# Kernel tuning notes

Measured on AMD Instinct MI355X. Metric: run time of the kernel, lower is better.

## Reference

```python
import jax, jax.numpy as jnp
import numpy as np

N = 50000          # num nodes
E = 800000         # num edges (before self loops)
IN_C = 128
HID = 256          # heads * head_dim
HEADS = 4
HEAD_DIM = HID // HEADS
OUT_C = 64
NEG_SLOPE = 0.2    # PyG GATConv default leaky_relu slope
BN_EPS = 1e-5


def _gat_conv(x, src, dst, W, att_src, att_dst, bias, concat):
    """PyG-style GATConv (with self loops already appended to src/dst).
    x: [N, in_c]; W: [in_c, H*C]; att_src/att_dst: [H, C]; bias: [H*C] or [C]."""
    H, C = att_src.shape
    h = (x @ W).reshape(-1, H, C)                               # [N, H, C]
    a_src = jnp.einsum('nhc,hc->nh', h, att_src)                # [N, H]
    a_dst = jnp.einsum('nhc,hc->nh', h, att_dst)                # [N, H]
    e = jax.nn.leaky_relu(a_src[src] + a_dst[dst], NEG_SLOPE)   # [Et, H]
    # segment softmax over destination nodes (numerically stable)
    m = jax.ops.segment_max(e, dst, num_segments=N)             # [N, H]
    m = jnp.where(jnp.isfinite(m), m, 0.0)
    ex = jnp.exp(e - m[dst])
    denom = jax.ops.segment_sum(ex, dst, num_segments=N)        # [N, H]
    alpha = ex / (denom[dst] + 1e-16)                           # [Et, H]
    msg = alpha[:, :, None] * h[src]                            # [Et, H, C]
    out = jax.ops.segment_sum(msg, dst, num_segments=N)         # [N, H, C]
    out = out.reshape(N, H * C) if concat else out.mean(axis=1)
    return out + bias


def _bn_eval(x, gamma, beta, mean, var):
    return (x - mean) * jax.lax.rsqrt(var + BN_EPS) * gamma + beta


def setup_inputs() -> dict:
    key = jax.random.key(0)
    ks = jax.random.split(key, 16)
    x = jax.random.normal(ks[0], (N, IN_C), dtype=jnp.float32)
    edge_index = jax.random.randint(ks[1], (2, E), 0, N, dtype=jnp.int64)

    def lin(k, fan_in, fan_out):
        s = (1.0 / np.sqrt(fan_in)).astype(np.float32)
        return jax.random.normal(k, (fan_in, fan_out), dtype=jnp.float32) * s

    def att(k, h, c):
        return jax.random.normal(k, (h, c), dtype=jnp.float32) * 0.1

    return {
        'x': x, 'edge_index': edge_index,
        'W0': lin(ks[2], IN_C, HID), 'as0': att(ks[3], HEADS, HEAD_DIM), 'ad0': att(ks[4], HEADS, HEAD_DIM), 'b0': jnp.zeros((HID,), jnp.float32),
        'bn0_g': jnp.ones((HID,), jnp.float32), 'bn0_b': jnp.zeros((HID,), jnp.float32), 'bn0_m': jnp.zeros((HID,), jnp.float32), 'bn0_v': jnp.ones((HID,), jnp.float32),
        'W1': lin(ks[5], HID, HID), 'as1': att(ks[6], HEADS, HEAD_DIM), 'ad1': att(ks[7], HEADS, HEAD_DIM), 'b1': jnp.zeros((HID,), jnp.float32),
        'bn1_g': jnp.ones((HID,), jnp.float32), 'bn1_b': jnp.zeros((HID,), jnp.float32), 'bn1_m': jnp.zeros((HID,), jnp.float32), 'bn1_v': jnp.ones((HID,), jnp.float32),
        'W2': lin(ks[8], HID, OUT_C), 'as2': att(ks[9], 1, OUT_C), 'ad2': att(ks[10], 1, OUT_C), 'b2': jnp.zeros((OUT_C,), jnp.float32),
    }


def reference(x, edge_index, W0, as0, ad0, b0, bn0_g, bn0_b, bn0_m, bn0_v,
              W1, as1, ad1, b1, bn1_g, bn1_b, bn1_m, bn1_v,
              W2, as2, ad2, b2):
    loop = jnp.arange(N, dtype=edge_index.dtype)
    src = jnp.concatenate([edge_index[0], loop])   # PyG add_self_loops=True
    dst = jnp.concatenate([edge_index[1], loop])

    h = _gat_conv(x, src, dst, W0, as0, ad0, b0, concat=True)
    h = jax.nn.elu(_bn_eval(h, bn0_g, bn0_b, bn0_m, bn0_v))   # dropout: eval -> identity
    h = _gat_conv(h, src, dst, W1, as1, ad1, b1, concat=True)
    h = jax.nn.elu(_bn_eval(h, bn1_g, bn1_b, bn1_m, bn1_v))
    out = _gat_conv(h, src, dst, W2, as2, ad2, b2, concat=False)  # heads=1, mean
    return out
```

## Files before the change

### kernel.cpp

```cpp
#include <hip/hip_runtime.h>

#define NN   50000
#define EE   800000
#define ET   850000
#define INC  128
#define HID  256
#define OUTC 64
#define NEG  0.2f
#define BNEPS 1e-5f

typedef __bf16 bf16x8 __attribute__((ext_vector_type(8)));
typedef float  f32x4  __attribute__((ext_vector_type(4)));

static __device__ __forceinline__ float b2f(unsigned short u) {
    return __uint_as_float(((unsigned)u) << 16);
}
static __device__ __forceinline__ float blo(unsigned u) {
    return __uint_as_float(u << 16);
}
static __device__ __forceinline__ float bhi(unsigned u) {
    return __uint_as_float(u & 0xFFFF0000u);
}
static __device__ __forceinline__ unsigned short f2b(float f) {
    unsigned u = __float_as_uint(f);
    unsigned r = u + 0x7FFFu + ((u >> 16) & 1u);
    return (unsigned short)(r >> 16);
}
static __device__ __forceinline__ float leaky(float x) {
    return x > 0.f ? x : NEG * x;
}
static __device__ __forceinline__ float ew(float e) {
    return __expf(fminf(e, 80.f));
}

__global__ void k_init(const int* __restrict__ ei, const unsigned* __restrict__ xw,
                       int* __restrict__ cnt, int* __restrict__ flagW, int* __restrict__ flagB,
                       int nbZ) {
    __shared__ int cs[4];
    int b = blockIdx.x, t = threadIdx.x;
    if (b < nbZ) {
        int i = b * 256 + t;
        if (i < NN) cnt[i] = 0;
    } else if (b == nbZ) {
        int c = 0;
        for (int k = 0; k < 16; k++) {
            int i = t + 256 * k;
            if (ei[2 * i + 1] != 0) c = 1;
        }
        for (int o = 1; o < 64; o <<= 1) c |= __shfl_xor(c, o);
        if ((t & 63) == 0) cs[t >> 6] = c;
        __syncthreads();
        if (t == 0) *flagW = cs[0] | cs[1] | cs[2] | cs[3];
    } else {
        int c = 0;
        for (int i = t; i < 4096; i += 256) {
            unsigned v = (xw[i] >> 8) & 0x7F;
            if (v >= 50 && v <= 67) c++;
        }
        for (int o = 1; o < 64; o <<= 1) c += __shfl_xor(c, o);
        if ((t & 63) == 0) cs[t >> 6] = c;
        __syncthreads();
        if (t == 0) *flagB = (cs[0] + cs[1] + cs[2] + cs[3] > 2048) ? 1 : 0;
    }
}

__global__ void k_prep(const void* as0, const void* ad0, const void* b0, const void* g0,
                       const void* be0, const void* m0, const void* v0,
                       const void* as1, const void* ad1, const void* b1, const void* g1,
                       const void* be1, const void* m1, const void* v1,
                       const void* as2, const void* ad2, const void* b2,
                       const void* W0, const void* W1, const void* W2,
                       unsigned short* __restrict__ WT0, unsigned short* __restrict__ WT1,
                       unsigned short* __restrict__ WT2,
                       const void* __restrict__ x, unsigned short* __restrict__ xb,
                       float* __restrict__ pp, const int* __restrict__ flagB) {
    int b = blockIdx.x, t = threadIdx.x;
    bool bf = (*flagB != 0);
    auto cv = [&](const void* s, int i) -> float {
        return bf ? b2f(((const unsigned short*)s)[i]) : ((const float*)s)[i];
    };
    if (b < 14) {
        float v;
        switch (b) {
            case 0:  v = cv(as0, t); break;
            case 1:  v = cv(ad0, t); break;
            case 2:  v = cv(b0, t);  break;
            case 3:  v = cv(g0, t);  break;
            case 4:  v = cv(be0, t); break;
            case 5:  v = cv(m0, t);  break;
            case 6:  v = cv(v0, t);  break;
            case 7:  v = cv(as1, t); break;
            case 8:  v = cv(ad1, t); break;
            case 9:  v = cv(b1, t);  break;
            case 10: v = cv(g1, t);  break;
            case 11: v = cv(be1, t); break;
            case 12: v = cv(m1, t);  break;
            default: v = cv(v1, t);  break;
        }
        pp[b * 256 + t] = v;
    } else if (b == 14) {
        if (t < 192) {
            int arr = t >> 6, j = t & 63;
            float v = (arr == 0) ? cv(as2, j) : (arr == 1) ? cv(ad2, j) : cv(b2, j);
            pp[14 * 256 + arr * 64 + j] = v;
        }
    } else if (b < 15 + 128) {
        int i = (b - 15) * 256 + t;
        int k = i >> 8, n = i & 255;
        WT0[n * INC + k] = bf ? ((const unsigned short*)W0)[i] : f2b(((const float*)W0)[i]);
    } else if (b < 15 + 128 + 256) {
        int i = (b - 143) * 256 + t;
        int k = i >> 8, n = i & 255;
        WT1[n * HID + k] = bf ? ((const unsigned short*)W1)[i] : f2b(((const float*)W1)[i]);
    } else if (b < 15 + 128 + 256 + 64) {
        int i = (b - 399) * 256 + t;
        int k = i >> 6, n = i & 63;
        WT2[n * HID + k] = bf ? ((const unsigned short*)W2)[i] : f2b(((const float*)W2)[i]);
    } else {
        if (bf) return;
        for (int i = (b - 463) * 256 + t; i < NN * INC; i += 2048 * 256)
            xb[i] = f2b(((const float*)x)[i]);
    }
}

__global__ void k_hist(const int* __restrict__ ei, const int* __restrict__ flagW,
                       int* __restrict__ cnt) {
    int i = blockIdx.x * 256 + threadIdx.x;
    if (i >= ET) return;
    bool w32 = (*flagW != 0);
    int d = (i < EE) ? (w32 ? ei[EE + i] : ei[2 * (EE + i)]) : (i - EE);
    atomicAdd(&cnt[d], 1);
}

static __device__ __forceinline__ int block_scan_incl(int v, int t, int* ws) {
    int lane = t & 63, w = t >> 6;
    int x = v;
    for (int o = 1; o < 64; o <<= 1) {
        int y = __shfl_up(x, o);
        if (lane >= o) x += y;
    }
    if (lane == 63) ws[w] = x;
    __syncthreads();
    if (t == 0) {
        int s = 0;
        for (int k = 0; k < 4; k++) { int tmp = ws[k]; ws[k] = s; s += tmp; }
    }
    __syncthreads();
    return x + ws[w];
}

__global__ void k_scan_a(const int* __restrict__ cnt, int* __restrict__ rowptr, int* __restrict__ bsum) {
    __shared__ int ws[4];
    int t = threadIdx.x, b = blockIdx.x;
    int i = b * 256 + t;
    int v = (i < NN) ? cnt[i] : 0;
    int incl = block_scan_incl(v, t, ws);
    if (i < NN) rowptr[i] = incl - v;
    if (t == 255) bsum[b] = incl;
}

__global__ void k_scan_b(int* __restrict__ bsum, int nb) {
    __shared__ int ws[4];
    int t = threadIdx.x;
    int v = (t < nb) ? bsum[t] : 0;
    int incl = block_scan_incl(v, t, ws);
    if (t < nb) bsum[t] = incl - v;
}

__global__ void k_scan_c(int* __restrict__ rowptr, const int* __restrict__ bsum, int* __restrict__ cursor) {
    int t = threadIdx.x, b = blockIdx.x;
    int i = b * 256 + t;
    if (i < NN) {
        int r = rowptr[i] + bsum[b];
        rowptr[i] = r;
        cursor[i] = r;
    }
    if (i == 0) rowptr[NN] = ET;
}

__global__ void k_scatter(const int* __restrict__ ei, const int* __restrict__ flagW,
                          int* __restrict__ cursor, int* __restrict__ esrc) {
    int i = blockIdx.x * 256 + threadIdx.x;
    if (i >= ET) {
        if (i < ET + 64) esrc[i] = 0;
        return;
    }
    bool w32 = (*flagW != 0);
    int s, d;
    if (i < EE) {
        if (w32) { s = ei[i];     d = ei[EE + i]; }
        else     { s = ei[2 * i]; d = ei[2 * (EE + i)]; }
    } else {
        s = d = i - EE;
    }
    int p = atomicAdd(&cursor[d], 1);
    esrc[p] = s;
}

template<int NC, int NH, int NBN>
__global__ __launch_bounds__(256) void k_gemm(const unsigned short* __restrict__ Amain,
                                              const void* __restrict__ Aalt,
                                              const int* __restrict__ flagB,
                                              const unsigned short* __restrict__ WT,
                                              unsigned short* __restrict__ H,
                                              float* __restrict__ asrc, float* __restrict__ adst,
                                              const float* __restrict__ asv, const float* __restrict__ adv,
                                              int M, int K) {
    constexpr int BN = 64 * NBN;
    __shared__ __align__(16) unsigned short As[128 * 40];
    __shared__ __align__(16) unsigned short Bs[BN * 40];
    const unsigned short* A = (*flagB) ? (const unsigned short*)Aalt : Amain;
    int t = threadIdx.x;
    int bm = blockIdx.x, bg = blockIdx.y;
    int lane = t & 63, wave = t >> 6;
    int m16 = lane & 15, quad = lane >> 4;

    f32x4 acc[2][4 * NBN];
    #pragma unroll
    for (int a = 0; a < 2; a++)
        #pragma unroll
        for (int b = 0; b < 4 * NBN; b++) acc[a][b] = (f32x4){0.f, 0.f, 0.f, 0.f};

    int arow = t >> 1, ahalf = t & 1;
    long gArow = (long)bm * 128 + arow;

    for (int k0 = 0; k0 < K; k0 += 32) {
        uint4 av0 = {0u, 0u, 0u, 0u}, av1 = {0u, 0u, 0u, 0u};
        if (gArow < M) {
            const unsigned short* ap = A + gArow * (size_t)K + k0 + ahalf * 16;
            av0 = *(const uint4*)(ap);
            av1 = *(const uint4*)(ap + 8);
        }
        if constexpr (NBN == 2) {
            const unsigned short* bp = WT + ((size_t)bg * BN + arow) * K + k0 + ahalf * 16;
            uint4 bv0 = *(const uint4*)(bp);
            uint4 bv1 = *(const uint4*)(bp + 8);
            *(uint4*)&As[arow * 40 + ahalf * 16]     = av0;
            *(uint4*)&As[arow * 40 + ahalf * 16 + 8] = av1;
            *(uint4*)&Bs[arow * 40 + ahalf * 16]     = bv0;
            *(uint4*)&Bs[arow * 40 + ahalf * 16 + 8] = bv1;
        } else {
            int brow = t >> 2, bq = t & 3;
            uint4 bv = *(const uint4*)(WT + ((size_t)bg * BN + brow) * K + k0 + bq * 8);
            *(uint4*)&As[arow * 40 + ahalf * 16]     = av0;
            *(uint4*)&As[arow * 40 + ahalf * 16 + 8] = av1;
            *(uint4*)&Bs[brow * 40 + bq * 8]         = bv;
        }
        __syncthreads();
        int wrow = wave * 32;
        bf16x8 af[2], bf[4 * NBN];
        #pragma unroll
        for (int mt = 0; mt < 2; mt++)
            af[mt] = *(const bf16x8*)&As[(wrow + mt * 16 + m16) * 40 + quad * 8];
        #pragma unroll
        for (int nt = 0; nt < 4 * NBN; nt++)
            bf[nt] = *(const bf16x8*)&Bs[(nt * 16 + m16) * 40 + quad * 8];
        #pragma unroll
        for (int mt = 0; mt < 2; mt++)
            #pragma unroll
            for (int nt = 0; nt < 4 * NBN; nt++)
                acc[mt][nt] = __builtin_amdgcn_mfma_f32_16x16x32_bf16(af[mt], bf[nt], acc[mt][nt], 0, 0, 0);
        __syncthreads();
    }

    float asc[4 * NBN], adc[4 * NBN];
    #pragma unroll
    for (int nt = 0; nt < 4 * NBN; nt++) {
        int col = bg * BN + nt * 16 + m16;
        asc[nt] = asv[col];
        adc[nt] = adv[col];
    }
    #pragma unroll
    for (int mt = 0; mt < 2; mt++) {
        int gR0 = bm * 128 + wave * 32 + mt * 16 + quad * 4;
        #pragma unroll
        for (int r = 0; r < 4; r++) {
            int gR = gR0 + r;
            #pragma unroll
            for (int hh = 0; hh < NBN; hh++) {
                float ps = 0.f, pd = 0.f;
                #pragma unroll
                for (int nt = hh * 4; nt < hh * 4 + 4; nt++) {
                    float v = acc[mt][nt][r];
                    ps += v * asc[nt];
                    pd += v * adc[nt];
                }
                for (int o = 1; o < 16; o <<= 1) { ps += __shfl_xor(ps, o); pd += __shfl_xor(pd, o); }
                if (m16 == 0 && gR < M) {
                    asrc[(size_t)gR * NH + bg * NBN + hh] = ps;
                    adst[(size_t)gR * NH + bg * NBN + hh] = pd;
                }
            }
            if (gR < M) {
                #pragma unroll
                for (int nt = 0; nt < 4 * NBN; nt++) {
                    int gC = bg * BN + nt * 16 + m16;
                    H[(size_t)gR * NC + gC] = f2b(acc[mt][nt][r]);
                }
            }
        }
    }
}

#define LOADG(pre, d, e0n) \
    uint2 pre##0 = {0, 0}, pre##1 = {0, 0}, pre##2 = {0, 0}, pre##3 = {0, 0}; \
    if (d) { \
        int s0_ = esrc[(e0n)], s1_ = esrc[(e0n) + 1], s2_ = esrc[(e0n) + 2], s3_ = esrc[(e0n) + 3]; \
        pre##0 = *(const uint2*)(h + (size_t)s0_ * HID + lc); \
        pre##1 = *(const uint2*)(h + (size_t)s1_ * HID + lc); \
        pre##2 = *(const uint2*)(h + (size_t)s2_ * HID + lc); \
        pre##3 = *(const uint2*)(h + (size_t)s3_ * HID + lc); \
    }
#define FMAG(pre, d, wreg, A0, A1, A2, A3, j) \
    if (d) { \
        float w0_ = __shfl(wreg, wsel + (j)),     w1_ = __shfl(wreg, wsel + (j) + 1); \
        float w2_ = __shfl(wreg, wsel + (j) + 2), w3_ = __shfl(wreg, wsel + (j) + 3); \
        A0 += w0_ * blo((pre##0).x) + w1_ * blo((pre##1).x) + w2_ * blo((pre##2).x) + w3_ * blo((pre##3).x); \
        A1 += w0_ * bhi((pre##0).x) + w1_ * bhi((pre##1).x) + w2_ * bhi((pre##2).x) + w3_ * bhi((pre##3).x); \
        A2 += w0_ * blo((pre##0).y) + w1_ * blo((pre##1).y) + w2_ * blo((pre##2).y) + w3_ * blo((pre##3).y); \
        A3 += w0_ * bhi((pre##0).y) + w1_ * bhi((pre##1).y) + w2_ * bhi((pre##2).y) + w3_ * bhi((pre##3).y); \
    }

__global__ __launch_bounds__(256, 4) void k_agg4(const unsigned short* __restrict__ h,
                       const float* __restrict__ asrc, const float* __restrict__ adst,
                       const int* __restrict__ rowptr, const int* __restrict__ esrc,
                       const float* __restrict__ bias,
                       const float* __restrict__ bng, const float* __restrict__ bnb,
                       const float* __restrict__ bnm, const float* __restrict__ bnv,
                       unsigned short* __restrict__ act) {
    int t = threadIdx.x;
    int wave = t >> 6, lane = t & 63;
    int nodeA = blockIdx.x * 8 + wave * 2;
    if (nodeA >= NN) return;
    int nodeB = nodeA + 1;
    bool hasB = (nodeB < NN);

    int hd = lane >> 4, li = lane & 15;
    int wsel = lane & 48;
    const size_t lc = (size_t)lane * 4;

    int e0A = __builtin_amdgcn_readfirstlane(rowptr[nodeA]);
    int e1A = __builtin_amdgcn_readfirstlane(rowptr[nodeA + 1]);
    int degA = e1A - e0A;
    int e0B = e1A, degB = 0;
    if (hasB) degB = __builtin_amdgcn_readfirstlane(rowptr[nodeB + 1]) - e1A;

    float adhA = adst[(size_t)nodeA * 4 + hd];
    float adhB = hasB ? adst[(size_t)nodeB * 4 + hd] : 0.f;

    float waccA = 0.f, waccB = 0.f;
    float aA0 = 0.f, aA1 = 0.f, aA2 = 0.f, aA3 = 0.f;
    float aB0 = 0.f, aB1 = 0.f, aB2 = 0.f, aB3 = 0.f;

    int nA = min(16, degA), nB = min(16, degB);
    float eA = 0.f, eB = 0.f;
    if (li < nA) { int s = esrc[e0A + li]; eA = asrc[(size_t)s * 4 + hd]; }
    if (li < nB) { int s = esrc[e0B + li]; eB = asrc[(size_t)s * 4 + hd]; }

    int degM = max(degA, degB);
    for (int c = 0; c < degM; c += 16) {
        float wA = (li < nA) ? ew(leaky(eA + adhA)) : 0.f;
        float wB = (li < nB) ? ew(leaky(eB + adhB)) : 0.f;
        waccA += wA; waccB += wB;
        int nA2 = min(16, degA - (c + 16));
        int nB2 = min(16, degB - (c + 16));
        eA = 0.f; eB = 0.f;
        if (li < nA2) { int s = esrc[e0A + c + 16 + li]; eA = asrc[(size_t)s * 4 + hd]; }
        if (li < nB2) { int s = esrc[e0B + c + 16 + li]; eB = asrc[(size_t)s * 4 + hd]; }
        bool dA0 = 0 < nA, dA1 = 4 < nA, dA2 = 8 < nA, dA3 = 12 < nA;
        bool dB0 = 0 < nB, dB1 = 4 < nB, dB2 = 8 < nB, dB3 = 12 < nB;
        LOADG(gA0, dA0, e0A + c)
        LOADG(gA1, dA1, e0A + c + 4)
        LOADG(gA2, dA2, e0A + c + 8)
        LOADG(gA3, dA3, e0A + c + 12)
        LOADG(gB0, dB0, e0B + c)
        LOADG(gB1, dB1, e0B + c + 4)
        LOADG(gB2, dB2, e0B + c + 8)
        LOADG(gB3, dB3, e0B + c + 12)
        FMAG(gA0, dA0, wA, aA0, aA1, aA2, aA3, 0)
        FMAG(gA1, dA1, wA, aA0, aA1, aA2, aA3, 4)
        FMAG(gA2, dA2, wA, aA0, aA1, aA2, aA3, 8)
        FMAG(gA3, dA3, wA, aA0, aA1, aA2, aA3, 12)
        FMAG(gB0, dB0, wB, aB0, aB1, aB2, aB3, 0)
        FMAG(gB1, dB1, wB, aB0, aB1, aB2, aB3, 4)
        FMAG(gB2, dB2, wB, aB0, aB1, aB2, aB3, 8)
        FMAG(gB3, dB3, wB, aB0, aB1, aB2, aB3, 12)
        nA = nA2; nB = nB2;
    }
    waccA += __shfl_xor(waccA, 1); waccA += __shfl_xor(waccA, 2);
    waccA += __shfl_xor(waccA, 4); waccA += __shfl_xor(waccA, 8);
    waccB += __shfl_xor(waccB, 1); waccB += __shfl_xor(waccB, 2);
    waccB += __shfl_xor(waccB, 4); waccB += __shfl_xor(waccB, 8);
    float invA = 1.f / (waccA + 1e-16f);
    float invB = 1.f / (waccB + 1e-16f);

    int c0 = lane * 4;
    float4 bi = *(const float4*)(bias + c0);
    float4 bm_ = *(const float4*)(bnm + c0);
    float4 bv_ = *(const float4*)(bnv + c0);
    float4 bg_ = *(const float4*)(bng + c0);
    float4 bb_ = *(const float4*)(bnb + c0);
    float sc[4], sh[4];
    {
        const float* bvp = (const float*)&bv_;
        const float* bgp = (const float*)&bg_;
        const float* bmp = (const float*)&bm_;
        const float* bbp = (const float*)&bb_;
        const float* bip = (const float*)&bi;
        #pragma unroll
        for (int jj = 0; jj < 4; jj++) {
            float s_ = rsqrtf(bvp[jj] + BNEPS) * bgp[jj];
            sc[jj] = s_;
            sh[jj] = bbp[jj] + (bip[jj] - bmp[jj]) * s_;
        }
    }
    {
        float o[4] = {aA0 * invA, aA1 * invA, aA2 * invA, aA3 * invA};
        unsigned short res[4];
        #pragma unroll
        for (int jj = 0; jj < 4; jj++) {
            float val = o[jj] * sc[jj] + sh[jj];
            val = val > 0.f ? val : expm1f(val);
            res[jj] = f2b(val);
        }
        *(ushort4*)(act + (size_t)nodeA * HID + c0) = *(ushort4*)res;
    }
    if (hasB) {
        float o[4] = {aB0 * invB, aB1 * invB, aB2 * invB, aB3 * invB};
        unsigned short res[4];
        #pragma unroll
        for (int jj = 0; jj < 4; jj++) {
            float val = o[jj] * sc[jj] + sh[jj];
            val = val > 0.f ? val : expm1f(val);
            res[jj] = f2b(val);
        }
        *(ushort4*)(act + (size_t)nodeB * HID + c0) = *(ushort4*)res;
    }
}

__global__ void k_agg1(const unsigned short* __restrict__ h,
                       const float* __restrict__ asrc, const float* __restrict__ adst,
                       const int* __restrict__ rowptr, const int* __restrict__ esrc,
                       const float* __restrict__ bias,
                       void* __restrict__ outp, const int* __restrict__ flagB) {
    int t = threadIdx.x;
    int wave = t >> 6, lane = t & 63;
    int node0 = blockIdx.x * 16 + wave * 4;
    int q = lane >> 4, lq = lane & 15;
    int qs = lane & 48;
    int node = node0 + q;
    const size_t lc4 = (size_t)lq * 4;

    int e0  = rowptr[node];
    int deg = rowptr[node + 1] - e0;
    float ad = adst[node];

    float den = 0.f;
    float a0 = 0.f, a1 = 0.f, a2 = 0.f, a3 = 0.f;

    int n = min(16, deg);
    int s = 0; float e = 0.f;
    if (lq < n) { s = esrc[e0 + lq]; e = asrc[s]; }

    int degM = deg;
    degM = max(degM, __shfl_xor(degM, 16));
    degM = max(degM, __shfl_xor(degM, 32));

    for (int c = 0; c < degM; c += 16) {
        float w = (lq < n) ? ew(leaky(e + ad)) : 0.f;
        den += w;
        int n2 = min(16, deg - (c + 16));
        int sN = 0; float eN = 0.f;
        if (lq < n2) { sN = esrc[e0 + c + 16 + lq]; eN = asrc[sN]; }
        #pragma unroll
        for (int g = 0; g < 4; g++) {
            int j = g * 4;
            if (j < n) {
                int s0 = __shfl(s, qs + j),     s1 = __shfl(s, qs + j + 1);
                int s2 = __shfl(s, qs + j + 2), s3 = __shfl(s, qs + j + 3);
                float w0 = __shfl(w, qs + j),     w1 = __shfl(w, qs + j + 1);
                float w2 = __shfl(w, qs + j + 2), w3 = __shfl(w, qs + j + 3);
                uint2 v0 = *(const uint2*)(h + (size_t)s0 * OUTC + lc4);
                uint2 v1 = *(const uint2*)(h + (size_t)s1 * OUTC + lc4);
                uint2 v2 = *(const uint2*)(h + (size_t)s2 * OUTC + lc4);
                uint2 v3 = *(const uint2*)(h + (size_t)s3 * OUTC + lc4);
                a0 += w0 * blo(v0.x) + w1 * blo(v1.x) + w2 * blo(v2.x) + w3 * blo(v3.x);
                a1 += w0 * bhi(v0.x) + w1 * bhi(v1.x) + w2 * bhi(v2.x) + w3 * bhi(v3.x);
                a2 += w0 * blo(v0.y) + w1 * blo(v1.y) + w2 * blo(v2.y) + w3 * blo(v3.y);
                a3 += w0 * bhi(v0.y) + w1 * bhi(v1.y) + w2 * bhi(v2.y) + w3 * bhi(v3.y);
            }
        }
        s = sN; e = eN; n = n2;
    }
    den += __shfl_xor(den, 1); den += __shfl_xor(den, 2);
    den += __shfl_xor(den, 4); den += __shfl_xor(den, 8);
    float inv = 1.f / (den + 1e-16f);
    int c0 = lq * 4;
    float v0 = a0 * inv + bias[c0];
    float v1 = a1 * inv + bias[c0 + 1];
    float v2 = a2 * inv + bias[c0 + 2];
    float v3 = a3 * inv + bias[c0 + 3];
    if (*flagB) {
        unsigned r0 = (unsigned)f2b(v0) | ((unsigned)f2b(v1) << 16);
        unsigned r1 = (unsigned)f2b(v2) | ((unsigned)f2b(v3) << 16);
        uint2 rv = {r0, r1};
        *(uint2*)((unsigned short*)outp + (size_t)node * OUTC + c0) = rv;
    } else {
        float4 rv = {v0, v1, v2, v3};
        *(float4*)((float*)outp + (size_t)node * OUTC + c0) = rv;
    }
}

extern "C" void kernel_launch(void* const* d_in, const int* in_sizes, int n_in,
                              void* d_out, int out_size, void* d_ws, size_t ws_size,
                              hipStream_t stream) {
    const void* x  = d_in[0];
    const int*  ei = (const int*)d_in[1];
    const void* W0 = d_in[2];
    const void* W1 = d_in[10];
    const void* W2 = d_in[18];

    char* ws = (char*)d_ws;
    size_t off = 0;
    auto alloc = [&](size_t n) { void* p = ws + off; off += (n + 255) & ~(size_t)255; return p; };

    unsigned short* xb  = (unsigned short*)alloc((size_t)NN * INC * 2);
    unsigned short* h   = (unsigned short*)alloc((size_t)NN * HID * 2);
    unsigned short* act = (unsigned short*)alloc((size_t)NN * HID * 2);
    unsigned short* WT0 = (unsigned short*)alloc((size_t)HID * INC * 2);
    unsigned short* WT1 = (unsigned short*)alloc((size_t)HID * HID * 2);
    unsigned short* WT2 = (unsigned short*)alloc((size_t)OUTC * HID * 2);
    float*          pp  = (float*)alloc((size_t)(14 * 256 + 3 * 64) * 4);
    float*  asrc   = (float*)alloc((size_t)NN * 4 * 4);
    float*  adst   = (float*)alloc((size_t)NN * 4 * 4);
    int*    cnt    = (int*)alloc((size_t)(NN + 2) * 4);
    int*    rowptr = (int*)alloc((size_t)(NN + 1) * 4);
    int*    cursor = (int*)alloc((size_t)NN * 4);
    int*    esrc   = (int*)alloc((size_t)(ET + 64) * 4);
    int*    bsum   = (int*)alloc(256 * 4);
    int*    flagW  = cnt + NN;
    int*    flagB  = cnt + NN + 1;

    float* P0 = pp;
    float* P1 = pp + 7 * 256;
    float* P2 = pp + 14 * 256;

    const int nbN = (NN + 255) / 256;
    const int nbE = (ET + 255) / 256;
    const int nbA4 = (NN + 7) / 8;
    const int nbA1 = NN / 16;
    const int nbPrep = 463 + 2048;
    dim3 gemmGrid0((NN + 127) / 128, HID / 128);
    dim3 gemmGrid2((NN + 127) / 128, 1);

    k_init<<<nbN + 2, 256, 0, stream>>>(ei, (const unsigned*)x, cnt, flagW, flagB, nbN);
    k_hist<<<nbE, 256, 0, stream>>>(ei, flagW, cnt);
    k_scan_a<<<nbN, 256, 0, stream>>>(cnt, rowptr, bsum);
    k_scan_b<<<1, 256, 0, stream>>>(bsum, nbN);
    k_scan_c<<<nbN, 256, 0, stream>>>(rowptr, bsum, cursor);
    k_scatter<<<nbE, 256, 0, stream>>>(ei, flagW, cursor, esrc);

    k_prep<<<nbPrep, 256, 0, stream>>>(d_in[3], d_in[4], d_in[5], d_in[6], d_in[7], d_in[8], d_in[9],
                                       d_in[11], d_in[12], d_in[13], d_in[14], d_in[15], d_in[16], d_in[17],
                                       d_in[19], d_in[20], d_in[21],
                                       W0, W1, W2, WT0, WT1, WT2, x, xb, pp, flagB);

    k_gemm<HID, 4, 2><<<gemmGrid0, 256, 0, stream>>>(xb, x, flagB, WT0, h, asrc, adst,
                                                     P0 + 0, P0 + 256, NN, INC);
    k_agg4<<<nbA4, 256, 0, stream>>>(h, asrc, adst, rowptr, esrc,
                                     P0 + 512, P0 + 768, P0 + 1024, P0 + 1280, P0 + 1536, act);

    k_gemm<HID, 4, 2><<<gemmGrid0, 256, 0, stream>>>(act, act, flagB, WT1, h, asrc, adst,
                                                     P1 + 0, P1 + 256, NN, HID);
    k_agg4<<<nbA4, 256, 0, stream>>>(h, asrc, adst, rowptr, esrc,
                                     P1 + 512, P1 + 768, P1 + 1024, P1 + 1280, P1 + 1536, act);

    k_gemm<OUTC, 1, 1><<<gemmGrid2, 256, 0, stream>>>(act, act, flagB, WT2, h, asrc, adst,
                                                      P2 + 0, P2 + 64, NN, HID);
    k_agg1<<<nbA1, 256, 0, stream>>>(h, asrc, adst, rowptr, esrc, P2 + 128, d_out, flagB);
}
```

Before: 434.7 us.

## Fuse graph-build kernels with prep and first GEMM to cut launches

Histogram and weight/input prep are merged into one kernel, and the three-kernel scan is replaced by a single 1024-thread block that scans 49 counts per thread. The edge scatter now runs in the same launch as the first-layer GEMM, which does not depend on the CSR. Histogram and scatter handle two edges per thread with vector loads. This cuts kernel launches and lets independent work overlap, but the single-block serial scan may be slow, and the scatter's atomics now compete with GEMM blocks.

```diff
diff --git a/kernel.cpp b/kernel.cpp
--- a/kernel.cpp
+++ b/kernel.cpp
@@ -64,7 +64,30 @@
     }
 }
 
-__global__ void k_prep(const void* as0, const void* ad0, const void* b0, const void* g0,
+static __device__ __forceinline__ void hist_body(int b, const int* __restrict__ ei,
+                                                 const int* __restrict__ flagW,
+                                                 int* __restrict__ cnt) {
+    int j = b * 256 + threadIdx.x;
+    int i0 = 2 * j;
+    if (i0 >= ET) return;
+    int d0, d1;
+    if (i0 < EE) {
+        if (*flagW) {
+            uint2 dv = *(const uint2*)(ei + EE + i0);
+            d0 = dv.x; d1 = dv.y;
+        } else {
+            uint4 dv = *(const uint4*)(ei + 2 * (EE + i0));
+            d0 = dv.x; d1 = dv.z;
+        }
+    } else {
+        d0 = i0 - EE; d1 = i0 + 1 - EE;
+    }
+    atomicAdd(&cnt[d0], 1);
+    atomicAdd(&cnt[d1], 1);
+}
+
+static __device__ void prep_body(int b,
+                       const void* as0, const void* ad0, const void* b0, const void* g0,
                        const void* be0, const void* m0, const void* v0,
                        const void* as1, const void* ad1, const void* b1, const void* g1,
                        const void* be1, const void* m1, const void* v1,
@@ -74,7 +97,7 @@
                        unsigned short* __restrict__ WT2,
                        const void* __restrict__ x, unsigned short* __restrict__ xb,
                        float* __restrict__ pp, const int* __restrict__ flagB) {
-    int b = blockIdx.x, t = threadIdx.x;
+    int t = threadIdx.x;
     bool bf = (*flagB != 0);
     auto cv = [&](const void* s, int i) -> float {
         return bf ? b2f(((const unsigned short*)s)[i]) : ((const float*)s)[i];
@@ -123,18 +146,39 @@
     }
 }
 
-__global__ void k_hist(const int* __restrict__ ei, const int* __restrict__ flagW,
-                       int* __restrict__ cnt) {
-    int i = blockIdx.x * 256 + threadIdx.x;
-    if (i >= ET) return;
-    bool w32 = (*flagW != 0);
-    int d = (i < EE) ? (w32 ? ei[EE + i] : ei[2 * (EE + i)]) : (i - EE);
-    atomicAdd(&cnt[d], 1);
-}
-
-static __device__ __forceinline__ int block_scan_incl(int v, int t, int* ws) {
+#define NB_HIST 1661
+__global__ __launch_bounds__(256) void k_histprep(
+                       const int* __restrict__ ei, const int* __restrict__ flagW,
+                       int* __restrict__ cnt,
+                       const void* as0, const void* ad0, const void* b0, const void* g0,
+                       const void* be0, const void* m0, const void* v0,
+                       const void* as1, const void* ad1, const void* b1, const void* g1,
+                       const void* be1, const void* m1, const void* v1,
+                       const void* as2, const void* ad2, const void* b2,
+                       const void* W0, const void* W1, const void* W2,
+                       unsigned short* __restrict__ WT0, unsigned short* __restrict__ WT1,
+                       unsigned short* __restrict__ WT2,
+                       const void* __restrict__ x, unsigned short* __restrict__ xb,
+                       float* __restrict__ pp, const int* __restrict__ flagB) {
+    int b = blockIdx.x;
+    if (b < NB_HIST) hist_body(b, ei, flagW, cnt);
+    else prep_body(b - NB_HIST, as0, ad0, b0, g0, be0, m0, v0,
+                   as1, ad1, b1, g1, be1, m1, v1, as2, ad2, b2,
+                   W0, W1, W2, WT0, WT1, WT2, x, xb, pp, flagB);
+}
+
+__global__ __launch_bounds__(1024) void k_scan(const int* __restrict__ cnt,
+                                               int* __restrict__ rowptr,
+                                               int* __restrict__ cursor) {
+    __shared__ int ws[16];
+    int t = threadIdx.x;
     int lane = t & 63, w = t >> 6;
-    int x = v;
+    const int PER = 49;
+    int base = t * PER;
+    int lim = min(base + PER, NN);
+    int sum = 0;
+    for (int i = base; i < lim; i++) sum += cnt[i];
+    int x = sum;
     for (int o = 1; o < 64; o <<= 1) {
         int y = __shfl_up(x, o);
         if (lane >= o) x += y;
@@ -143,75 +187,60 @@
     __syncthreads();
     if (t == 0) {
         int s = 0;
-        for (int k = 0; k < 4; k++) { int tmp = ws[k]; ws[k] = s; s += tmp; }
+        for (int k = 0; k < 16; k++) { int tmp = ws[k]; ws[k] = s; s += tmp; }
     }
     __syncthreads();
-    return x + ws[w];
-}
-
-__global__ void k_scan_a(const int* __restrict__ cnt, int* __restrict__ rowptr, int* __restrict__ bsum) {
-    __shared__ int ws[4];
-    int t = threadIdx.x, b = blockIdx.x;
-    int i = b * 256 + t;
-    int v = (i < NN) ? cnt[i] : 0;
-    int incl = block_scan_incl(v, t, ws);
-    if (i < NN) rowptr[i] = incl - v;
-    if (t == 255) bsum[b] = incl;
-}
-
-__global__ void k_scan_b(int* __restrict__ bsum, int nb) {
-    __shared__ int ws[4];
-    int t = threadIdx.x;
-    int v = (t < nb) ? bsum[t] : 0;
-    int incl = block_scan_incl(v, t, ws);
-    if (t < nb) bsum[t] = incl - v;
-}
-
-__global__ void k_scan_c(int* __restrict__ rowptr, const int* __restrict__ bsum, int* __restrict__ cursor) {
-    int t = threadIdx.x, b = blockIdx.x;
-    int i = b * 256 + t;
-    if (i < NN) {
-        int r = rowptr[i] + bsum[b];
-        rowptr[i] = r;
-        cursor[i] = r;
-    }
-    if (i == 0) rowptr[NN] = ET;
-}
-
-__global__ void k_scatter(const int* __restrict__ ei, const int* __restrict__ flagW,
-                          int* __restrict__ cursor, int* __restrict__ esrc) {
-    int i = blockIdx.x * 256 + threadIdx.x;
-    if (i >= ET) {
-        if (i < ET + 64) esrc[i] = 0;
+    int run = ws[w] + (x - sum);
+    for (int i = base; i < lim; i++) {
+        int v = cnt[i];
+        rowptr[i] = run;
+        cursor[i] = run;
+        run += v;
+    }
+    if (t == 1023) rowptr[NN] = ET;
+}
+
+static __device__ __forceinline__ void scatter_body(int b, const int* __restrict__ ei,
+                                                    const int* __restrict__ flagW,
+                                                    int* __restrict__ cursor,
+                                                    int* __restrict__ esrc) {
+    int j = b * 256 + threadIdx.x;
+    int i0 = 2 * j;
+    if (i0 >= ET + 64) return;
+    if (i0 >= ET) {
+        esrc[i0] = 0;
+        if (i0 + 1 < ET + 64) esrc[i0 + 1] = 0;
         return;
     }
-    bool w32 = (*flagW != 0);
-    int s, d;
-    if (i < EE) {
-        if (w32) { s = ei[i];     d = ei[EE + i]; }
-        else     { s = ei[2 * i]; d = ei[2 * (EE + i)]; }
+    int s0, d0, s1, d1;
+    if (i0 < EE) {
+        if (*flagW) {
+            uint2 sv = *(const uint2*)(ei + i0);
+            uint2 dv = *(const uint2*)(ei + EE + i0);
+            s0 = sv.x; s1 = sv.y; d0 = dv.x; d1 = dv.y;
+        } else {
+            uint4 sv = *(const uint4*)(ei + 2 * i0);
+            uint4 dv = *(const uint4*)(ei + 2 * (EE + i0));
+            s0 = sv.x; s1 = sv.z; d0 = dv.x; d1 = dv.z;
+        }
     } else {
-        s = d = i - EE;
-    }
-    int p = atomicAdd(&cursor[d], 1);
-    esrc[p] = s;
+        s0 = d0 = i0 - EE; s1 = d1 = i0 + 1 - EE;
+    }
+    int p0 = atomicAdd(&cursor[d0], 1); esrc[p0] = s0;
+    int p1 = atomicAdd(&cursor[d1], 1); esrc[p1] = s1;
 }
 
 template<int NC, int NH, int NBN>
-__global__ __launch_bounds__(256) void k_gemm(const unsigned short* __restrict__ Amain,
-                                              const void* __restrict__ Aalt,
-                                              const int* __restrict__ flagB,
-                                              const unsigned short* __restrict__ WT,
-                                              unsigned short* __restrict__ H,
-                                              float* __restrict__ asrc, float* __restrict__ adst,
-                                              const float* __restrict__ asv, const float* __restrict__ adv,
-                                              int M, int K) {
+static __device__ void gemm_body(int bm, int bg, const unsigned short* __restrict__ A,
+                                 const unsigned short* __restrict__ WT,
+                                 unsigned short* __restrict__ H,
+                                 float* __restrict__ asrc, float* __restrict__ adst,
+                                 const float* __restrict__ asv, const float* __restrict__ adv,
+                                 int M, int K) {
     constexpr int BN = 64 * NBN;
     __shared__ __align__(16) unsigned short As[128 * 40];
     __shared__ __align__(16) unsigned short Bs[BN * 40];
-    const unsigned short* A = (*flagB) ? (const unsigned short*)Aalt : Amain;
     int t = threadIdx.x;
-    int bm = blockIdx.x, bg = blockIdx.y;
     int lane = t & 63, wave = t >> 6;
     int m16 = lane & 15, quad = lane >> 4;
 
@@ -299,6 +328,36 @@
                 }
             }
         }
+    }
+}
+
+template<int NC, int NH, int NBN>
+__global__ __launch_bounds__(256) void k_gemm(const unsigned short* __restrict__ Amain,
+                                              const void* __restrict__ Aalt,
+                                              const int* __restrict__ flagB,
+                                              const unsigned short* __restrict__ WT,
+                                              unsigned short* __restrict__ H,
+                                              float* __restrict__ asrc, float* __restrict__ adst,
+                                              const float* __restrict__ asv, const float* __restrict__ adv,
+                                              int M, int K) {
+    const unsigned short* A = (*flagB) ? (const unsigned short*)Aalt : Amain;
+    gemm_body<NC, NH, NBN>(blockIdx.x, blockIdx.y, A, WT, H, asrc, adst, asv, adv, M, K);
+}
+
+#define NB_G0 (((NN + 127) / 128) * 2)
+__global__ __launch_bounds__(256) void k_scatgemm0(
+        const int* __restrict__ ei, const int* __restrict__ flagW,
+        int* __restrict__ cursor, int* __restrict__ esrc,
+        const unsigned short* __restrict__ Amain, const void* __restrict__ Aalt,
+        const int* __restrict__ flagB, const unsigned short* __restrict__ WT,
+        unsigned short* __restrict__ H, float* __restrict__ asrc, float* __restrict__ adst,
+        const float* __restrict__ asv, const float* __restrict__ adv) {
+    int b = blockIdx.x;
+    if (b < NB_G0) {
+        const unsigned short* A = (*flagB) ? (const unsigned short*)Aalt : Amain;
+        gemm_body<HID, 4, 2>(b >> 1, b & 1, A, WT, H, asrc, adst, asv, adv, NN, INC);
+    } else {
+        scatter_body(b - NB_G0, ei, flagW, cursor, esrc);
     }
 }
 
@@ -546,35 +605,29 @@
     float* P2 = pp + 14 * 256;
 
     const int nbN = (NN + 255) / 256;
-    const int nbE = (ET + 255) / 256;
+    const int nbHP = NB_HIST + 463 + 2048;
+    const int nbSG = NB_G0 + 1661;
     const int nbA4 = (NN + 7) / 8;
     const int nbA1 = NN / 16;
-    const int nbPrep = 463 + 2048;
-    dim3 gemmGrid0((NN + 127) / 128, HID / 128);
+    dim3 gemmGrid1((NN + 127) / 128, HID / 128);
     dim3 gemmGrid2((NN + 127) / 128, 1);
 
     k_init<<<nbN + 2, 256, 0, stream>>>(ei, (const unsigned*)x, cnt, flagW, flagB, nbN);
-    k_hist<<<nbE, 256, 0, stream>>>(ei, flagW, cnt);
-    k_scan_a<<<nbN, 256, 0, stream>>>(cnt, rowptr, bsum);
-    k_scan_b<<<1, 256, 0, stream>>>(bsum, nbN);
-    k_scan_c<<<nbN, 256, 0, stream>>>(rowptr, bsum, cursor);
-    k_scatter<<<nbE, 256, 0, stream>>>(ei, flagW, cursor, esrc);
-
-    k_prep<<<nbPrep, 256, 0, stream>>>(d_in[3], d_in[4], d_in[5], d_in[6], d_in[7], d_in[8], d_in[9],
-                                       d_in[11], d_in[12], d_in[13], d_in[14], d_in[15], d_in[16], d_in[17],
-                                       d_in[19], d_in[20], d_in[21],
-                                       W0, W1, W2, WT0, WT1, WT2, x, xb, pp, flagB);
-
-    k_gemm<HID, 4, 2><<<gemmGrid0, 256, 0, stream>>>(xb, x, flagB, WT0, h, asrc, adst,
-                                                     P0 + 0, P0 + 256, NN, INC);
+    k_histprep<<<nbHP, 256, 0, stream>>>(ei, flagW, cnt,
+                                         d_in[3], d_in[4], d_in[5], d_in[6], d_in[7], d_in[8], d_in[9],
+                                         d_in[11], d_in[12], d_in[13], d_in[14], d_in[15], d_in[16], d_in[17],
+                                         d_in[19], d_in[20], d_in[21],
+                                         W0, W1, W2, WT0, WT1, WT2, x, xb, pp, flagB);
+    k_scan<<<1, 1024, 0, stream>>>(cnt, rowptr, cursor);
+    k_scatgemm0<<<nbSG, 256, 0, stream>>>(ei, flagW, cursor, esrc,
+                                          xb, x, flagB, WT0, h, asrc, adst,
+                                          P0 + 0, P0 + 256);
     k_agg4<<<nbA4, 256, 0, stream>>>(h, asrc, adst, rowptr, esrc,
                                      P0 + 512, P0 + 768, P0 + 1024, P0 + 1280, P0 + 1536, act);
-
-    k_gemm<HID, 4, 2><<<gemmGrid0, 256, 0, stream>>>(act, act, flagB, WT1, h, asrc, adst,
+    k_gemm<HID, 4, 2><<<gemmGrid1, 256, 0, stream>>>(act, act, flagB, WT1, h, asrc, adst,
                                                      P1 + 0, P1 + 256, NN, HID);
     k_agg4<<<nbA4, 256, 0, stream>>>(h, asrc, adst, rowptr, esrc,
                                      P1 + 512, P1 + 768, P1 + 1024, P1 + 1280, P1 + 1536, act);
-
     k_gemm<OUTC, 1, 1><<<gemmGrid2, 256, 0, stream>>>(act, act, flagB, WT2, h, asrc, adst,
                                                       P2 + 0, P2 + 64, NN, HID);
     k_agg1<<<nbA1, 256, 0, stream>>>(h, asrc, adst, rowptr, esrc, P2 + 128, d_out, flagB);
```

After: 548.6 us. 26.2% more time.
